# Kernel optimization log

Hardware: AMD Instinct MI355X
Metric: run time of the kernel (lower is better)

## Reference

```python
import jax, jax.numpy as jnp
import numpy as np

N, K, D_IN, D_H, D_A, N_CLS = 8192, 10, 1024, 512, 256, 4


def setup_inputs() -> dict:
    key = jax.random.key(0)
    ks = jax.random.split(key, 20)
    def lin(k, fan_in, shape):
        return jax.random.normal(k, shape, dtype=jnp.float32) / np.sqrt(fan_in)
    return {
        "x_path": jax.random.normal(ks[0], (N, D_IN), dtype=jnp.float32),
        "cluster_id": jax.random.randint(ks[1], (N,), 0, K),
        # per-cluster phi MLP (Linear 1024->512, ReLU, Linear 512->512, ReLU); dropout = eval identity
        "W1": lin(ks[2], D_IN, (K, D_IN, D_H)), "b1": jnp.zeros((K, D_H), jnp.float32),
        "W2": lin(ks[3], D_H, (K, D_H, D_H)), "b2": jnp.zeros((K, D_H), jnp.float32),
        # attention_net fc: Linear 512->512 + ReLU
        "fc_W": lin(ks[4], D_H, (D_H, D_H)), "fc_b": jnp.zeros((D_H,), jnp.float32),
        # Attn_Net_Gated: a=tanh(Va), b=sigmoid(Vb), A=(a*b)@Vc
        "Va": lin(ks[5], D_H, (D_H, D_A)), "ba": jnp.zeros((D_A,), jnp.float32),
        "Vb": lin(ks[6], D_H, (D_H, D_A)), "bb": jnp.zeros((D_A,), jnp.float32),
        "Vc": lin(ks[7], D_A, (D_A, 1)), "bc": jnp.zeros((1,), jnp.float32),
        # rho: Linear 512->256 + ReLU
        "rho_W": lin(ks[8], D_H, (D_H, D_A)), "rho_b": jnp.zeros((D_A,), jnp.float32),
        # classifier: Linear 256->4
        "cls_W": lin(ks[9], D_A, (D_A, N_CLS)), "cls_b": jnp.zeros((N_CLS,), jnp.float32),
    }


def reference(x_path, cluster_id, W1, b1, W2, b2, fc_W, fc_b,
              Va, ba, Vb, bb, Vc, bc, rho_W, rho_b, cls_W, cls_b):
    # mask[k, n] = 1 if patch n belongs to cluster k
    mask = (cluster_id[None, :] == jnp.arange(K)[:, None]).astype(x_path.dtype)  # [K, N]

    # per-cluster 2-layer MLP applied to all patches, masked mean-pool (= AdaptiveAvgPool1d(1))
    def phi(W1i, b1i, W2i, b2i):
        h = jax.nn.relu(x_path @ W1i + b1i)          # [N, 512]
        return jax.nn.relu(h @ W2i + b2i)            # [N, 512]
    y = jax.vmap(phi)(W1, b1, W2, b2)                # [K, N, 512]
    cnt = mask.sum(axis=1)                           # [K]
    pooled = jnp.einsum('kn,knd->kd', mask, y) / jnp.maximum(cnt, 1.0)[:, None]  # [K, 512]
    # empty cluster -> zeros (matches torch.zeros((1,512)) branch since b terms are zero via where)
    pooled = jnp.where(cnt[:, None] > 0, pooled, 0.0)

    # attention_net: fc + gated attention
    h = jax.nn.relu(pooled @ fc_W + fc_b)            # [K, 512]
    a = jnp.tanh(h @ Va + ba)                        # [K, 256]
    b = jax.nn.sigmoid(h @ Vb + bb)                  # [K, 256]
    A = (a * b) @ Vc + bc                            # [K, 1]
    A = jax.nn.softmax(A.T, axis=1)                  # [1, K]
    h_path = A @ h                                   # [1, 512]
    h_path = jax.nn.relu(h_path @ rho_W + rho_b)[0]  # [256]
    logits = (h_path @ cls_W + cls_b)[None, :]       # [1, 4]
    Y_hat = jnp.argmax(logits, axis=1, keepdims=True)
    hazards = jax.nn.sigmoid(logits)
    S = jnp.cumprod(1.0 - hazards, axis=1)
    return hazards, S, Y_hat
```

## Files before the change

kernel.cpp:

```cpp
#include <hip/hip_runtime.h>
#include <math.h>

#define NPATCH 8192
#define KC     10
#define DIN    1024
#define DH     512
#define DA     256
#define NCLS   4

#define TM  32
#define LDA 520

typedef unsigned short u16;
typedef short bf16x8 __attribute__((ext_vector_type(8)));
typedef float f32x4  __attribute__((ext_vector_type(4)));

#define OFF_CNT   0
#define OFF_BAR   48
#define OFF_IDX   64
#define OFF_PSUM  327744
#define OFF_H     348224
#define OFF_H2    368768
#define OFF_SRED  369792
#define OFF_W1P   373888
#define OFF_W2P   10859648

__device__ __forceinline__ u16 f2bf(float f) {
  union { float f; unsigned u; } v; v.f = f;
  unsigned r = (v.u + 0x7fffu + ((v.u >> 16) & 1u)) >> 16;
  return (u16)r;
}

__device__ __forceinline__ unsigned cvtpk(float lo, float hi) {
  unsigned r;
  asm("v_cvt_pk_bf16_f32 %0, %1, %2" : "=v"(r) : "v"(lo), "v"(hi));
  return r;
}

struct __align__(8) U16x4 { u16 x, y, z, w; };
union BF8U { bf16x8 v; unsigned u[4]; };

#define W1_TILES (KC * (DIN / 32) * (DH / 32))
#define W2_TILES (KC * (DH / 32) * (DH / 32))
#define NB_BUCKET 32
#define WT_PER_BLK 4
#define NB_PREP (NB_BUCKET + (W1_TILES + W2_TILES) / WT_PER_BLK)

__global__ __launch_bounds__(256) void prep_kernel(
    const int* __restrict__ cid, int* __restrict__ cnt,
    int* __restrict__ idxlist, const float* __restrict__ W1,
    const float* __restrict__ W2, u16* __restrict__ W1p,
    u16* __restrict__ W2p, float* __restrict__ psum) {
  int b = blockIdx.x, t = threadIdx.x;
  if (b < NB_BUCKET) {
    int g = b * 256 + t;
    if (g < KC * DH) psum[g] = 0.f;
    __shared__ int lcnt[KC], lbase[KC];
    if (t < KC) lcnt[t] = 0;
    __syncthreads();
    int n = b * 256 + t;
    int k = cid[n];
    int myoff = atomicAdd(&lcnt[k], 1);
    __syncthreads();
    if (t < KC) lbase[t] = atomicAdd(&cnt[t], lcnt[t]);
    __syncthreads();
    idxlist[k * NPATCH + lbase[k] + myoff] = n;
  } else {
    __shared__ u16 tile[32][33];
#pragma unroll
    for (int it = 0; it < WT_PER_BLK; ++it) {
      int bb = (b - NB_BUCKET) * WT_PER_BLK + it;
      const float* src;
      u16* dst;
      if (bb < W1_TILES) {
        int k = bb / 512, rem = bb % 512;
        int kb = rem / 16, n0 = (rem % 16) * 32;
        src = W1 + (size_t)k * DIN * DH + (size_t)kb * 32 * DH + n0;
        dst = W1p + (((size_t)(k * 32 + kb) * 512 + n0) * 32);
      } else {
        int b2 = bb - W1_TILES;
        int k = b2 / 256, rem = b2 % 256;
        int kb = rem / 16, n0 = (rem % 16) * 32;
        src = W2 + (size_t)k * DH * DH + (size_t)kb * 32 * DH + n0;
        dst = W2p + (((size_t)(k * 16 + kb) * 512 + n0) * 32);
      }
      {
        int ki = t >> 3, n4 = (t & 7) * 4;
        float4 v = *(const float4*)&src[(size_t)ki * DH + n4];
        tile[ki][n4 + 0] = f2bf(v.x);
        tile[ki][n4 + 1] = f2bf(v.y);
        tile[ki][n4 + 2] = f2bf(v.z);
        tile[ki][n4 + 3] = f2bf(v.w);
      }
      __syncthreads();
      {
        int n = t >> 3, ki = (t & 7) * 4;
        U16x4 o = {tile[ki + 0][n], tile[ki + 1][n], tile[ki + 2][n],
                   tile[ki + 3][n]};
        *(U16x4*)&dst[(size_t)n * 32 + ki] = o;
      }
      __syncthreads();
    }
  }
}

__global__ __launch_bounds__(512, 4) void phi_kernel(
    const float* __restrict__ x, const u16* __restrict__ W1p,
    const u16* __restrict__ W2p, const float* __restrict__ b1,
    const float* __restrict__ b2, const int* __restrict__ cnt,
    const int* __restrict__ idxlist, float* __restrict__ psum) {
  __shared__ __align__(16) u16 A0[TM * LDA];
  __shared__ __align__(16) u16 A1[TM * LDA];
  __shared__ int ridx[TM];

  const int tid = threadIdx.x;
  const int w = tid >> 6, lane = tid & 63;
  const int quad = lane >> 4, l16 = lane & 15;

  int cn[KC];
#pragma unroll
  for (int i = 0; i < KC; ++i) cn[i] = cnt[i];
  int G = 0;
#pragma unroll
  for (int i = 0; i < KC; ++i) G += (cn[i] + TM - 1) >> 5;

  const int s = blockIdx.x & 7, j = blockIdx.x >> 3;
  const int lo = (G * s) >> 3, hi = (G * (s + 1)) >> 3;

  for (int g = lo + j; g < hi; g += 64) {
    int kk = 0, rg = g, cntk = cn[0];
#pragma unroll
    for (int i = 0; i < KC - 1; ++i) {
      int nch = (cn[i] + TM - 1) >> 5;
      if (rg >= nch) { kk = i + 1; rg -= nch; cntk = cn[i + 1]; }
    }
    const int base = rg * TM;

    if (tid < TM)
      ridx[tid] = (base + tid < cntk) ? idxlist[kk * NPATCH + base + tid] : -1;
    __syncthreads();

    const u16* wb = W1p + ((size_t)(kk * 32) * 512 + (w * 64 + l16)) * 32 +
                    quad * 8;
    bf16x8 B[3][4];
#pragma unroll
    for (int p = 0; p < 3; ++p)
#pragma unroll
      for (int nt = 0; nt < 4; ++nt)
        B[p][nt] = *(const bf16x8*)(wb + (size_t)p * 16384 + nt * 512);

#pragma unroll
    for (int u8 = 0; u8 < 8; ++u8) {
      const int kh = u8 & 1;
      const int r = w * 4 + (u8 >> 1);
      int src = ridx[r];
      BF8U o;
      if (src >= 0) {
        const float4* xp =
            (const float4*)(x + (size_t)src * DIN + kh * 512 + lane * 8);
        float4 v0 = xp[0], v1 = xp[1];
        o.u[0] = cvtpk(v0.x, v0.y);
        o.u[1] = cvtpk(v0.z, v0.w);
        o.u[2] = cvtpk(v1.x, v1.y);
        o.u[3] = cvtpk(v1.z, v1.w);
      } else {
        o.u[0] = 0; o.u[1] = 0; o.u[2] = 0; o.u[3] = 0;
      }
      u16* dstbuf = kh ? A1 : A0;
      *(bf16x8*)&dstbuf[r * LDA + lane * 8] = o.v;
    }
    __syncthreads();

    const f32x4 zero4 = {0.f, 0.f, 0.f, 0.f};
    f32x4 acc[2][4];
#pragma unroll
    for (int m = 0; m < 2; ++m)
#pragma unroll
      for (int nt = 0; nt < 4; ++nt) acc[m][nt] = zero4;

#pragma unroll
    for (int ks = 0; ks < 32; ++ks) {
      const int cur = ks % 3;
      const u16* Abuf = (ks < 16) ? A0 : A1;
      const int ao = (ks & 15) * 32 + quad * 8;
      bf16x8 af0 = *(const bf16x8*)&Abuf[l16 * LDA + ao];
      bf16x8 af1 = *(const bf16x8*)&Abuf[(16 + l16) * LDA + ao];
#pragma unroll
      for (int nt = 0; nt < 4; ++nt) {
        acc[0][nt] = __builtin_amdgcn_mfma_f32_16x16x32_bf16(
            af0, B[cur][nt], acc[0][nt], 0, 0, 0);
        acc[1][nt] = __builtin_amdgcn_mfma_f32_16x16x32_bf16(
            af1, B[cur][nt], acc[1][nt], 0, 0, 0);
      }
      if (ks < 29) {
#pragma unroll
        for (int nt = 0; nt < 4; ++nt)
          B[cur][nt] =
              *(const bf16x8*)(wb + (size_t)(ks + 3) * 16384 + nt * 512);
      }
    }

    const u16* wb2 = W2p + ((size_t)(kk * 16) * 512 + (w * 64 + l16)) * 32 +
                     quad * 8;
#pragma unroll
    for (int p = 0; p < 3; ++p)
#pragma unroll
      for (int nt = 0; nt < 4; ++nt)
        B[p][nt] = *(const bf16x8*)(wb2 + (size_t)p * 16384 + nt * 512);

    __syncthreads();

#pragma unroll
    for (int m = 0; m < 2; ++m)
#pragma unroll
      for (int nt = 0; nt < 4; ++nt) {
        int c = w * 64 + nt * 16 + l16;
        float bias = b1[kk * DH + c];
#pragma unroll
        for (int r = 0; r < 4; ++r) {
          int row = m * 16 + quad * 4 + r;
          A0[row * LDA + c] = f2bf(fmaxf(acc[m][nt][r] + bias, 0.f));
        }
      }
    __syncthreads();

    f32x4 acc2[2][4];
#pragma unroll
    for (int m = 0; m < 2; ++m)
#pragma unroll
      for (int nt = 0; nt < 4; ++nt) acc2[m][nt] = zero4;

#pragma unroll
    for (int ks = 0; ks < 16; ++ks) {
      const int cur = ks % 3;
      const int ao = ks * 32 + quad * 8;
      bf16x8 af0 = *(const bf16x8*)&A0[l16 * LDA + ao];
      bf16x8 af1 = *(const bf16x8*)&A0[(16 + l16) * LDA + ao];
#pragma unroll
      for (int nt = 0; nt < 4; ++nt) {
        acc2[0][nt] = __builtin_amdgcn_mfma_f32_16x16x32_bf16(
            af0, B[cur][nt], acc2[0][nt], 0, 0, 0);
        acc2[1][nt] = __builtin_amdgcn_mfma_f32_16x16x32_bf16(
            af1, B[cur][nt], acc2[1][nt], 0, 0, 0);
      }
      if (ks < 13) {
#pragma unroll
        for (int nt = 0; nt < 4; ++nt)
          B[cur][nt] =
              *(const bf16x8*)(wb2 + (size_t)(ks + 3) * 16384 + nt * 512);
      }
    }

    float vmask[2][4];
#pragma unroll
    for (int m = 0; m < 2; ++m)
#pragma unroll
      for (int r = 0; r < 4; ++r)
        vmask[m][r] = (base + m * 16 + quad * 4 + r < cntk) ? 1.f : 0.f;

#pragma unroll
    for (int nt = 0; nt < 4; ++nt) {
      int col = w * 64 + nt * 16 + l16;
      float bias = b2[kk * DH + col];
      float sv = 0.f;
#pragma unroll
      for (int m = 0; m < 2; ++m)
#pragma unroll
        for (int r = 0; r < 4; ++r)
          sv += vmask[m][r] * fmaxf(acc2[m][nt][r] + bias, 0.f);
      sv += __shfl_xor(sv, 16, 64);
      sv += __shfl_xor(sv, 32, 64);
      if (quad == 0) atomicAdd(&psum[kk * DH + col], sv);
    }
  }
}

#define NTB 64

__device__ __forceinline__ void bar_arrive_wait(int* bar) {
  __syncthreads();
  if (threadIdx.x == 0) {
    __threadfence();
    __hip_atomic_fetch_add(bar, 1, __ATOMIC_RELEASE, __HIP_MEMORY_SCOPE_AGENT);
    while (__hip_atomic_load(bar, __ATOMIC_ACQUIRE,
                             __HIP_MEMORY_SCOPE_AGENT) < NTB) {
      __builtin_amdgcn_s_sleep(1);
    }
  }
  __syncthreads();
}

__global__ __launch_bounds__(256) void tail_kernel(
    const float* __restrict__ psum, const int* __restrict__ cnt,
    const float* __restrict__ fcW, const float* __restrict__ fcb,
    const float* __restrict__ Va, const float* __restrict__ ba,
    const float* __restrict__ Vb, const float* __restrict__ bb_,
    const float* __restrict__ Vc, const float* __restrict__ rhoW,
    const float* __restrict__ rhob, const float* __restrict__ clsW,
    const float* __restrict__ clsb, float* __restrict__ hstore,
    float* __restrict__ sred, float* __restrict__ h2g,
    int* __restrict__ bar, float* __restrict__ out) {
  __shared__ float p_sh[KC * DH];
  __shared__ float r1[2560];
  __shared__ float r2[2560];
  __shared__ float invs[KC];
  __shared__ float gate_sh[4 * KC];
  __shared__ float ws_sh[KC];
  __shared__ float hp_sh[DH];
  const int tid = threadIdx.x;
  const int b = blockIdx.x;

  if (tid < KC) {
    int c = cnt[tid];
    invs[tid] = (c > 0) ? 1.f / (float)c : 0.f;
  }
  __syncthreads();
#pragma unroll
  for (int it = 0; it < KC * DH / 256; ++it) {
    int e = it * 256 + tid;
    p_sh[e] = psum[e] * invs[e >> 9];
  }
  __syncthreads();
  {
    const int jj = tid & 7, dq = tid >> 3;
    const int j0 = b * 8;
    float acc[KC];
#pragma unroll
    for (int k = 0; k < KC; ++k) acc[k] = 0.f;
#pragma unroll 4
    for (int i = 0; i < 16; ++i) {
      int d = dq * 16 + i;
      float wv = fcW[(size_t)d * DH + j0 + jj];
#pragma unroll
      for (int k = 0; k < KC; ++k) acc[k] = fmaf(p_sh[k * DH + d], wv, acc[k]);
    }
#pragma unroll
    for (int k = 0; k < KC; ++k) r1[(dq * 8 + jj) * KC + k] = acc[k];
    __syncthreads();
    if (tid < 8 * KC) {
      int jj2 = tid / KC, k = tid % KC;
      float s = 0.f;
#pragma unroll
      for (int q = 0; q < 32; ++q) s += r1[(q * 8 + jj2) * KC + k];
      hstore[k * DH + j0 + jj2] = fmaxf(s + fcb[j0 + jj2], 0.f);
    }
  }
  bar_arrive_wait(&bar[0]);

#pragma unroll
  for (int it = 0; it < KC * DH / 256; ++it) {
    int e = it * 256 + tid;
    p_sh[e] = hstore[e];
  }
  __syncthreads();
  {
    const int jj = tid & 3, dq = tid >> 2;
    const int j0 = b * 4;
    float sa[KC], sb[KC];
#pragma unroll
    for (int k = 0; k < KC; ++k) { sa[k] = 0.f; sb[k] = 0.f; }
#pragma unroll 4
    for (int i = 0; i < 8; ++i) {
      int d = dq * 8 + i;
      float va = Va[(size_t)d * DA + j0 + jj];
      float vb = Vb[(size_t)d * DA + j0 + jj];
#pragma unroll
      for (int k = 0; k < KC; ++k) {
        float h = p_sh[k * DH + d];
        sa[k] = fmaf(h, va, sa[k]);
        sb[k] = fmaf(h, vb, sb[k]);
      }
    }
#pragma unroll
    for (int k = 0; k < KC; ++k) {
      r1[(dq * 4 + jj) * KC + k] = sa[k];
      r2[(dq * 4 + jj) * KC + k] = sb[k];
    }
    __syncthreads();
    if (tid < 4 * KC) {
      int jj2 = tid / KC, k = tid % KC;
      float ta = 0.f, tb = 0.f;
#pragma unroll
      for (int q = 0; q < 64; ++q) {
        ta += r1[(q * 4 + jj2) * KC + k];
        tb += r2[(q * 4 + jj2) * KC + k];
      }
      float a = tanhf(ta + ba[j0 + jj2]);
      float g = 1.f / (1.f + expf(-(tb + bb_[j0 + jj2])));
      gate_sh[jj2 * KC + k] = a * g * Vc[j0 + jj2];
    }
    __syncthreads();
    if (tid < KC) {
      float s = 0.f;
#pragma unroll
      for (int jj2 = 0; jj2 < 4; ++jj2) s += gate_sh[jj2 * KC + tid];
      sred[b * 16 + tid] = s;
    }
  }
  bar_arrive_wait(&bar[1]);

  if (tid < KC) {
    float s = 0.f;
    for (int q = 0; q < NTB; ++q) s += sred[q * 16 + tid];
    ws_sh[tid] = s;
  }
  __syncthreads();
  if (tid == 0) {
    float m = -1e30f;
#pragma unroll
    for (int k2 = 0; k2 < KC; ++k2) m = fmaxf(m, ws_sh[k2]);
    float Z = 0.f;
#pragma unroll
    for (int k2 = 0; k2 < KC; ++k2) {
      float e = expf(ws_sh[k2] - m);
      ws_sh[k2] = e;
      Z += e;
    }
    float iZ = 1.f / Z;
#pragma unroll
    for (int k2 = 0; k2 < KC; ++k2) ws_sh[k2] *= iZ;
  }
  __syncthreads();
#pragma unroll
  for (int it = 0; it < 2; ++it) {
    int d = it * 256 + tid;
    float s = 0.f;
#pragma unroll
    for (int k2 = 0; k2 < KC; ++k2) s = fmaf(ws_sh[k2], p_sh[k2 * DH + d], s);
    hp_sh[d] = s;
  }
  __syncthreads();
  {
    const int jj = tid & 3, dq = tid >> 2;
    const int j0 = b * 4;
    float acc = 0.f;
#pragma unroll 4
    for (int i = 0; i < 8; ++i) {
      int d = dq * 8 + i;
      acc = fmaf(hp_sh[d], rhoW[(size_t)d * DA + j0 + jj], acc);
    }
    r1[dq * 4 + jj] = acc;
    __syncthreads();
    if (tid < 4) {
      float s = 0.f;
#pragma unroll
      for (int q = 0; q < 64; ++q) s += r1[q * 4 + tid];
      h2g[j0 + tid] = fmaxf(s + rhob[j0 + tid], 0.f);
    }
  }

  if (b != 0) {
    __syncthreads();
    if (tid == 0) {
      __threadfence();
      __hip_atomic_fetch_add(&bar[2], 1, __ATOMIC_RELEASE,
                             __HIP_MEMORY_SCOPE_AGENT);
    }
    return;
  }
  bar_arrive_wait(&bar[2]);
  {
    float h = h2g[tid];
#pragma unroll
    for (int c = 0; c < NCLS; ++c)
      r1[c * 256 + tid] = h * clsW[(size_t)tid * NCLS + c];
    __syncthreads();
    for (int s = 128; s > 0; s >>= 1) {
      if (tid < s) {
#pragma unroll
        for (int c = 0; c < NCLS; ++c)
          r1[c * 256 + tid] += r1[c * 256 + tid + s];
      }
      __syncthreads();
    }
    if (tid == 0) {
      float lg[NCLS], hz[NCLS];
      int best = 0;
#pragma unroll
      for (int c = 0; c < NCLS; ++c) {
        lg[c] = r1[c * 256] + clsb[c];
        hz[c] = 1.f / (1.f + expf(-lg[c]));
        if (lg[c] > lg[best]) best = c;
      }
      float S = 1.f;
#pragma unroll
      for (int c = 0; c < NCLS; ++c) out[c] = hz[c];
#pragma unroll
      for (int c = 0; c < NCLS; ++c) {
        S *= (1.f - hz[c]);
        out[NCLS + c] = S;
      }
      out[2 * NCLS] = (float)best;
    }
  }
}

extern "C" void kernel_launch(void* const* d_in, const int* in_sizes, int n_in,
                              void* d_out, int out_size, void* d_ws,
                              size_t ws_size, hipStream_t stream) {
  const float* x    = (const float*)d_in[0];
  const int*   cid  = (const int*)d_in[1];
  const float* W1   = (const float*)d_in[2];
  const float* b1   = (const float*)d_in[3];
  const float* W2   = (const float*)d_in[4];
  const float* b2   = (const float*)d_in[5];
  const float* fcW  = (const float*)d_in[6];
  const float* fcb  = (const float*)d_in[7];
  const float* Va   = (const float*)d_in[8];
  const float* ba   = (const float*)d_in[9];
  const float* Vb   = (const float*)d_in[10];
  const float* bb_  = (const float*)d_in[11];
  const float* Vc   = (const float*)d_in[12];
  const float* rhoW = (const float*)d_in[14];
  const float* rhob = (const float*)d_in[15];
  const float* clsW = (const float*)d_in[16];
  const float* clsb = (const float*)d_in[17];
  float* out = (float*)d_out;

  char* ws = (char*)d_ws;
  int*   cnt     = (int*)(ws + OFF_CNT);
  int*   bar     = (int*)(ws + OFF_BAR);
  int*   idxlist = (int*)(ws + OFF_IDX);
  float* psum    = (float*)(ws + OFF_PSUM);
  float* hstore  = (float*)(ws + OFF_H);
  float* h2g     = (float*)(ws + OFF_H2);
  float* sred    = (float*)(ws + OFF_SRED);
  u16*   W1p     = (u16*)(ws + OFF_W1P);
  u16*   W2p     = (u16*)(ws + OFF_W2P);

  (void)hipMemsetAsync(cnt, 0, 64, stream);
  prep_kernel<<<NB_PREP, 256, 0, stream>>>(cid, cnt, idxlist, W1, W2, W1p, W2p,
                                           psum);
  phi_kernel<<<512, 512, 0, stream>>>(x, W1p, W2p, b1, b2, cnt, idxlist, psum);
  tail_kernel<<<NTB, 256, 0, stream>>>(psum, cnt, fcW, fcb, Va, ba, Vb, bb_,
                                       Vc, rhoW, rhob, clsW, clsb, hstore,
                                       sred, h2g, bar, out);
}
```

Measured before the change: 205.9 us.

## Stream phi weights via global_load_lds double buffer with swizzled LDS and rotated K order

Replaces the register-resident triple-buffered weight prefetch with direct global-to-LDS DMA (global_load_lds) into per-wave double buffers, using explicit vmcnt/lgkmcnt waits. The padded activation tiles become XOR-swizzled unpadded layouts, and each group starts the K loop at a group-dependent rotation to spread weight reads across blocks. It aims to cut VGPR pressure, which is why the occupancy hint in launch bounds is removed, and to overlap weight fetches with MFMA. The cost is extra LDS traffic and use and hand-tuned wait counts, which could be fragile.

```diff
diff --git a/kernel.cpp b/kernel.cpp
--- a/kernel.cpp
+++ b/kernel.cpp
@@ -9,7 +9,6 @@
 #define NCLS   4
 
 #define TM  32
-#define LDA 520
 
 typedef unsigned short u16;
 typedef short bf16x8 __attribute__((ext_vector_type(8)));
@@ -39,6 +38,12 @@
 
 struct __align__(8) U16x4 { u16 x, y, z, w; };
 union BF8U { bf16x8 v; unsigned u[4]; };
+
+__device__ __forceinline__ void dma16(const u16* gp, u16* lp) {
+  __builtin_amdgcn_global_load_lds(
+      (const __attribute__((address_space(1))) void*)gp,
+      (__attribute__((address_space(3))) void*)lp, 16, 0, 0);
+}
 
 #define W1_TILES (KC * (DIN / 32) * (DH / 32))
 #define W2_TILES (KC * (DH / 32) * (DH / 32))
@@ -104,19 +109,23 @@
   }
 }
 
-__global__ __launch_bounds__(512, 4) void phi_kernel(
+__global__ __launch_bounds__(512) void phi_kernel(
     const float* __restrict__ x, const u16* __restrict__ W1p,
     const u16* __restrict__ W2p, const float* __restrict__ b1,
     const float* __restrict__ b2, const int* __restrict__ cnt,
     const int* __restrict__ idxlist, float* __restrict__ psum) {
-  __shared__ __align__(16) u16 A0[TM * LDA];
-  __shared__ __align__(16) u16 A1[TM * LDA];
-  __shared__ int ridx[TM];
+  __shared__ __align__(16) u16 A0[TM * 512];
+  __shared__ __align__(16) u16 A1[TM * 512];
+  __shared__ __align__(16) u16 Bsh[2 * 8 * 4 * 512];
 
   const int tid = threadIdx.x;
   const int w = tid >> 6, lane = tid & 63;
   const int quad = lane >> 4, l16 = lane & 15;
 
+  const int boff = (w * 64 + l16) * 32 + quad * 8;
+  u16* myB0 = &Bsh[(size_t)w * 2048];
+  u16* myB1 = &Bsh[16384 + (size_t)w * 2048];
+
   int cn[KC];
 #pragma unroll
   for (int i = 0; i < KC; ++i) cn[i] = cnt[i];
@@ -135,27 +144,18 @@
       if (rg >= nch) { kk = i + 1; rg -= nch; cntk = cn[i + 1]; }
     }
     const int base = rg * TM;
-
-    if (tid < TM)
-      ridx[tid] = (base + tid < cntk) ? idxlist[kk * NPATCH + base + tid] : -1;
-    __syncthreads();
-
-    const u16* wb = W1p + ((size_t)(kk * 32) * 512 + (w * 64 + l16)) * 32 +
-                    quad * 8;
-    bf16x8 B[3][4];
-#pragma unroll
-    for (int p = 0; p < 3; ++p)
-#pragma unroll
-      for (int nt = 0; nt < 4; ++nt)
-        B[p][nt] = *(const bf16x8*)(wb + (size_t)p * 16384 + nt * 512);
+    const int rot = (g * 5) & 31;
+    const int rot2 = (g * 5) & 15;
+
+    __syncthreads();
 
 #pragma unroll
     for (int u8 = 0; u8 < 8; ++u8) {
       const int kh = u8 & 1;
       const int r = w * 4 + (u8 >> 1);
-      int src = ridx[r];
       BF8U o;
-      if (src >= 0) {
+      if (base + r < cntk) {
+        int src = idxlist[kk * NPATCH + base + r];
         const float4* xp =
             (const float4*)(x + (size_t)src * DIN + kh * 512 + lane * 8);
         float4 v0 = xp[0], v1 = xp[1];
@@ -167,9 +167,19 @@
         o.u[0] = 0; o.u[1] = 0; o.u[2] = 0; o.u[3] = 0;
       }
       u16* dstbuf = kh ? A1 : A0;
-      *(bf16x8*)&dstbuf[r * LDA + lane * 8] = o.v;
-    }
-    __syncthreads();
+      *(bf16x8*)&dstbuf[r * 512 + (lane ^ (r & 7)) * 8] = o.v;
+    }
+    __syncthreads();
+
+    const u16* w1base = W1p + (size_t)(kk * 32) * 16384 + boff;
+    const u16* w2base = W2p + (size_t)(kk * 16) * 16384 + boff;
+#pragma unroll
+    for (int p = 0; p < 2; ++p) {
+      const u16* sb = w1base + (size_t)(((p + rot) & 31)) * 16384;
+      u16* lb = p ? myB1 : myB0;
+#pragma unroll
+      for (int nt = 0; nt < 4; ++nt) dma16(sb + nt * 512, lb + nt * 512);
+    }
 
     const f32x4 zero4 = {0.f, 0.f, 0.f, 0.f};
     f32x4 acc[2][4];
@@ -179,35 +189,37 @@
       for (int nt = 0; nt < 4; ++nt) acc[m][nt] = zero4;
 
 #pragma unroll
-    for (int ks = 0; ks < 32; ++ks) {
-      const int cur = ks % 3;
-      const u16* Abuf = (ks < 16) ? A0 : A1;
-      const int ao = (ks & 15) * 32 + quad * 8;
-      bf16x8 af0 = *(const bf16x8*)&Abuf[l16 * LDA + ao];
-      bf16x8 af1 = *(const bf16x8*)&Abuf[(16 + l16) * LDA + ao];
+    for (int t = 0; t < 32; ++t) {
+      asm volatile("s_waitcnt vmcnt(4)" ::: "memory");
+      __builtin_amdgcn_sched_barrier(0);
+      const u16* mb = (t & 1) ? myB1 : myB0;
+      bf16x8 bf[4];
+#pragma unroll
+      for (int nt = 0; nt < 4; ++nt)
+        bf[nt] = *(const bf16x8*)(mb + nt * 512 + lane * 8);
+      const int ks = (t + rot) & 31;
+      const u16* Ab = (ks < 16) ? A0 : A1;
+      const int c8 = (((ks & 15) * 4 + quad) ^ (l16 & 7)) * 8;
+      bf16x8 af0 = *(const bf16x8*)&Ab[l16 * 512 + c8];
+      bf16x8 af1 = *(const bf16x8*)&Ab[(16 + l16) * 512 + c8];
+      asm volatile("s_waitcnt lgkmcnt(0)" ::: "memory");
+      __builtin_amdgcn_sched_barrier(0);
+      {
+        u16* lb = (t & 1) ? myB1 : myB0;
+        const u16* sb = (t < 30)
+            ? w1base + (size_t)(((t + 2 + rot) & 31)) * 16384
+            : w2base + (size_t)(((t - 30 + rot2) & 15)) * 16384;
+#pragma unroll
+        for (int nt = 0; nt < 4; ++nt) dma16(sb + nt * 512, lb + nt * 512);
+      }
 #pragma unroll
       for (int nt = 0; nt < 4; ++nt) {
         acc[0][nt] = __builtin_amdgcn_mfma_f32_16x16x32_bf16(
-            af0, B[cur][nt], acc[0][nt], 0, 0, 0);
+            af0, bf[nt], acc[0][nt], 0, 0, 0);
         acc[1][nt] = __builtin_amdgcn_mfma_f32_16x16x32_bf16(
-            af1, B[cur][nt], acc[1][nt], 0, 0, 0);
-      }
-      if (ks < 29) {
-#pragma unroll
-        for (int nt = 0; nt < 4; ++nt)
-          B[cur][nt] =
-              *(const bf16x8*)(wb + (size_t)(ks + 3) * 16384 + nt * 512);
-      }
-    }
-
-    const u16* wb2 = W2p + ((size_t)(kk * 16) * 512 + (w * 64 + l16)) * 32 +
-                     quad * 8;
-#pragma unroll
-    for (int p = 0; p < 3; ++p)
-#pragma unroll
-      for (int nt = 0; nt < 4; ++nt)
-        B[p][nt] = *(const bf16x8*)(wb2 + (size_t)p * 16384 + nt * 512);
-
+            af1, bf[nt], acc[1][nt], 0, 0, 0);
+      }
+    }
     __syncthreads();
 
 #pragma unroll
@@ -219,7 +231,8 @@
 #pragma unroll
         for (int r = 0; r < 4; ++r) {
           int row = m * 16 + quad * 4 + r;
-          A0[row * LDA + c] = f2bf(fmaxf(acc[m][nt][r] + bias, 0.f));
+          A0[row * 512 + (((c >> 3) ^ (row & 7)) * 8) + (c & 7)] =
+              f2bf(fmaxf(acc[m][nt][r] + bias, 0.f));
         }
       }
     __syncthreads();
@@ -231,23 +244,36 @@
       for (int nt = 0; nt < 4; ++nt) acc2[m][nt] = zero4;
 
 #pragma unroll
-    for (int ks = 0; ks < 16; ++ks) {
-      const int cur = ks % 3;
-      const int ao = ks * 32 + quad * 8;
-      bf16x8 af0 = *(const bf16x8*)&A0[l16 * LDA + ao];
-      bf16x8 af1 = *(const bf16x8*)&A0[(16 + l16) * LDA + ao];
+    for (int t = 0; t < 16; ++t) {
+      if (t == 15) {
+        asm volatile("s_waitcnt vmcnt(0)" ::: "memory");
+      } else {
+        asm volatile("s_waitcnt vmcnt(4)" ::: "memory");
+      }
+      __builtin_amdgcn_sched_barrier(0);
+      const u16* mb = (t & 1) ? myB1 : myB0;
+      bf16x8 bf[4];
+#pragma unroll
+      for (int nt = 0; nt < 4; ++nt)
+        bf[nt] = *(const bf16x8*)(mb + nt * 512 + lane * 8);
+      const int ks2 = (t + rot2) & 15;
+      const int c8 = ((ks2 * 4 + quad) ^ (l16 & 7)) * 8;
+      bf16x8 af0 = *(const bf16x8*)&A0[l16 * 512 + c8];
+      bf16x8 af1 = *(const bf16x8*)&A0[(16 + l16) * 512 + c8];
+      asm volatile("s_waitcnt lgkmcnt(0)" ::: "memory");
+      __builtin_amdgcn_sched_barrier(0);
+      if (t < 14) {
+        u16* lb = (t & 1) ? myB1 : myB0;
+        const u16* sb = w2base + (size_t)(((t + 2 + rot2) & 15)) * 16384;
+#pragma unroll
+        for (int nt = 0; nt < 4; ++nt) dma16(sb + nt * 512, lb + nt * 512);
+      }
 #pragma unroll
       for (int nt = 0; nt < 4; ++nt) {
         acc2[0][nt] = __builtin_amdgcn_mfma_f32_16x16x32_bf16(
-            af0, B[cur][nt], acc2[0][nt], 0, 0, 0);
+            af0, bf[nt], acc2[0][nt], 0, 0, 0);
         acc2[1][nt] = __builtin_amdgcn_mfma_f32_16x16x32_bf16(
-            af1, B[cur][nt], acc2[1][nt], 0, 0, 0);
-      }
-      if (ks < 13) {
-#pragma unroll
-        for (int nt = 0; nt < 4; ++nt)
-          B[cur][nt] =
-              *(const bf16x8*)(wb2 + (size_t)(ks + 3) * 16384 + nt * 512);
+            af1, bf[nt], acc2[1][nt], 0, 0, 0);
       }
     }
 
```

New measurement: 211.4 us. 1.03x slower.

## Pre-convert x to bf16 and DMA rows into LDS via global_load_lds

Applied to the files above, without the earlier changes.

The prep kernel gains a pass that converts x to bf16 in workspace, and the phi kernel loads activation rows straight into shared memory with global_load_lds instead of loading fp32 and converting in registers. The packed weight layout is reordered so each lane's 16-byte B fragment is contiguous across the wave, giving coalesced weight loads. Weight-packing blocks now handle one tile each instead of four. This adds an extra full read and write of x in prep, in exchange for halving the bytes phi reads for x and removing conversion work from the GEMM kernel.

```diff
diff --git a/kernel.cpp b/kernel.cpp
--- a/kernel.cpp
+++ b/kernel.cpp
@@ -24,6 +24,7 @@
 #define OFF_SRED  369792
 #define OFF_W1P   373888
 #define OFF_W2P   10859648
+#define OFF_XB    16102528
 
 __device__ __forceinline__ u16 f2bf(float f) {
   union { float f; unsigned u; } v; v.f = f;
@@ -31,26 +32,26 @@
   return (u16)r;
 }
 
-__device__ __forceinline__ unsigned cvtpk(float lo, float hi) {
-  unsigned r;
-  asm("v_cvt_pk_bf16_f32 %0, %1, %2" : "=v"(r) : "v"(lo), "v"(hi));
-  return r;
-}
-
 struct __align__(8) U16x4 { u16 x, y, z, w; };
-union BF8U { bf16x8 v; unsigned u[4]; };
+
+__device__ __forceinline__ void dma16(const u16* gp, void* lp) {
+  __builtin_amdgcn_global_load_lds(
+      (const __attribute__((address_space(1))) void*)gp,
+      (__attribute__((address_space(3))) void*)lp, 16, 0, 0);
+}
 
 #define W1_TILES (KC * (DIN / 32) * (DH / 32))
 #define W2_TILES (KC * (DH / 32) * (DH / 32))
 #define NB_BUCKET 32
-#define WT_PER_BLK 4
-#define NB_PREP (NB_BUCKET + (W1_TILES + W2_TILES) / WT_PER_BLK)
+#define NB_XB     2048
+#define NB_PREP (NB_BUCKET + NB_XB + W1_TILES + W2_TILES)
 
 __global__ __launch_bounds__(256) void prep_kernel(
     const int* __restrict__ cid, int* __restrict__ cnt,
     int* __restrict__ idxlist, const float* __restrict__ W1,
     const float* __restrict__ W2, u16* __restrict__ W1p,
-    u16* __restrict__ W2p, float* __restrict__ psum) {
+    u16* __restrict__ W2p, const float* __restrict__ x,
+    u16* __restrict__ xb, float* __restrict__ psum) {
   int b = blockIdx.x, t = threadIdx.x;
   if (b < NB_BUCKET) {
     int g = b * 256 + t;
@@ -65,47 +66,55 @@
     if (t < KC) lbase[t] = atomicAdd(&cnt[t], lcnt[t]);
     __syncthreads();
     idxlist[k * NPATCH + lbase[k] + myoff] = n;
+  } else if (b < NB_BUCKET + NB_XB) {
+    int cb = b - NB_BUCKET;
+    size_t basei = (size_t)cb * 4096;
+#pragma unroll
+    for (int i = 0; i < 4; ++i) {
+      size_t off = basei + (size_t)i * 1024 + (size_t)t * 4;
+      float4 v = *(const float4*)(x + off);
+      U16x4 o = {f2bf(v.x), f2bf(v.y), f2bf(v.z), f2bf(v.w)};
+      *(U16x4*)(xb + off) = o;
+    }
   } else {
     __shared__ u16 tile[32][33];
-#pragma unroll
-    for (int it = 0; it < WT_PER_BLK; ++it) {
-      int bb = (b - NB_BUCKET) * WT_PER_BLK + it;
-      const float* src;
-      u16* dst;
-      if (bb < W1_TILES) {
-        int k = bb / 512, rem = bb % 512;
-        int kb = rem / 16, n0 = (rem % 16) * 32;
-        src = W1 + (size_t)k * DIN * DH + (size_t)kb * 32 * DH + n0;
-        dst = W1p + (((size_t)(k * 32 + kb) * 512 + n0) * 32);
-      } else {
-        int b2 = bb - W1_TILES;
-        int k = b2 / 256, rem = b2 % 256;
-        int kb = rem / 16, n0 = (rem % 16) * 32;
-        src = W2 + (size_t)k * DH * DH + (size_t)kb * 32 * DH + n0;
-        dst = W2p + (((size_t)(k * 16 + kb) * 512 + n0) * 32);
-      }
-      {
-        int ki = t >> 3, n4 = (t & 7) * 4;
-        float4 v = *(const float4*)&src[(size_t)ki * DH + n4];
-        tile[ki][n4 + 0] = f2bf(v.x);
-        tile[ki][n4 + 1] = f2bf(v.y);
-        tile[ki][n4 + 2] = f2bf(v.z);
-        tile[ki][n4 + 3] = f2bf(v.w);
-      }
-      __syncthreads();
-      {
-        int n = t >> 3, ki = (t & 7) * 4;
-        U16x4 o = {tile[ki + 0][n], tile[ki + 1][n], tile[ki + 2][n],
-                   tile[ki + 3][n]};
-        *(U16x4*)&dst[(size_t)n * 32 + ki] = o;
-      }
-      __syncthreads();
+    int bb = b - NB_BUCKET - NB_XB;
+    const float* src;
+    u16* dst;
+    if (bb < W1_TILES) {
+      int k = bb / 512, rem = bb % 512;
+      int kb = rem / 16, n0 = (rem % 16) * 32;
+      src = W1 + (size_t)k * DIN * DH + (size_t)kb * 32 * DH + n0;
+      dst = W1p + (((size_t)(k * 32 + kb) * 512 + n0) * 32);
+    } else {
+      int b2 = bb - W1_TILES;
+      int k = b2 / 256, rem = b2 % 256;
+      int kb = rem / 16, n0 = (rem % 16) * 32;
+      src = W2 + (size_t)k * DH * DH + (size_t)kb * 32 * DH + n0;
+      dst = W2p + (((size_t)(k * 16 + kb) * 512 + n0) * 32);
+    }
+    {
+      int ki = t >> 3, n4 = (t & 7) * 4;
+      float4 v = *(const float4*)&src[(size_t)ki * DH + n4];
+      tile[ki][n4 + 0] = f2bf(v.x);
+      tile[ki][n4 + 1] = f2bf(v.y);
+      tile[ki][n4 + 2] = f2bf(v.z);
+      tile[ki][n4 + 3] = f2bf(v.w);
+    }
+    __syncthreads();
+    {
+      int n = t >> 3, ki = (t & 7) * 4;
+      U16x4 o = {tile[ki + 0][n], tile[ki + 1][n], tile[ki + 2][n],
+                 tile[ki + 3][n]};
+      size_t idx = (size_t)(n >> 4) * 512 + ((ki >> 3) * 128) +
+                   ((n & 15) * 8) + (ki & 7);
+      *(U16x4*)&dst[idx] = o;
     }
   }
 }
 
 __global__ __launch_bounds__(512, 4) void phi_kernel(
-    const float* __restrict__ x, const u16* __restrict__ W1p,
+    const u16* __restrict__ xb, const u16* __restrict__ W1p,
     const u16* __restrict__ W2p, const float* __restrict__ b1,
     const float* __restrict__ b2, const int* __restrict__ cnt,
     const int* __restrict__ idxlist, float* __restrict__ psum) {
@@ -140,8 +149,7 @@
       ridx[tid] = (base + tid < cntk) ? idxlist[kk * NPATCH + base + tid] : -1;
     __syncthreads();
 
-    const u16* wb = W1p + ((size_t)(kk * 32) * 512 + (w * 64 + l16)) * 32 +
-                    quad * 8;
+    const u16* wb = W1p + (size_t)(kk * 32) * 16384 + w * 2048 + lane * 8;
     bf16x8 B[3][4];
 #pragma unroll
     for (int p = 0; p < 3; ++p)
@@ -154,20 +162,14 @@
       const int kh = u8 & 1;
       const int r = w * 4 + (u8 >> 1);
       int src = ridx[r];
-      BF8U o;
+      u16* dstbuf = kh ? A1 : A0;
       if (src >= 0) {
-        const float4* xp =
-            (const float4*)(x + (size_t)src * DIN + kh * 512 + lane * 8);
-        float4 v0 = xp[0], v1 = xp[1];
-        o.u[0] = cvtpk(v0.x, v0.y);
-        o.u[1] = cvtpk(v0.z, v0.w);
-        o.u[2] = cvtpk(v1.x, v1.y);
-        o.u[3] = cvtpk(v1.z, v1.w);
+        dma16(xb + (size_t)src * DIN + kh * 512 + lane * 8,
+              &dstbuf[r * LDA]);
       } else {
-        o.u[0] = 0; o.u[1] = 0; o.u[2] = 0; o.u[3] = 0;
-      }
-      u16* dstbuf = kh ? A1 : A0;
-      *(bf16x8*)&dstbuf[r * LDA + lane * 8] = o.v;
+        bf16x8 z = {0, 0, 0, 0, 0, 0, 0, 0};
+        *(bf16x8*)&dstbuf[r * LDA + lane * 8] = z;
+      }
     }
     __syncthreads();
 
@@ -179,10 +181,10 @@
       for (int nt = 0; nt < 4; ++nt) acc[m][nt] = zero4;
 
 #pragma unroll
-    for (int ks = 0; ks < 32; ++ks) {
-      const int cur = ks % 3;
-      const u16* Abuf = (ks < 16) ? A0 : A1;
-      const int ao = (ks & 15) * 32 + quad * 8;
+    for (int t = 0; t < 32; ++t) {
+      const int cur = t % 3;
+      const u16* Abuf = (t < 16) ? A0 : A1;
+      const int ao = (t & 15) * 32 + quad * 8;
       bf16x8 af0 = *(const bf16x8*)&Abuf[l16 * LDA + ao];
       bf16x8 af1 = *(const bf16x8*)&Abuf[(16 + l16) * LDA + ao];
 #pragma unroll
@@ -192,16 +194,15 @@
         acc[1][nt] = __builtin_amdgcn_mfma_f32_16x16x32_bf16(
             af1, B[cur][nt], acc[1][nt], 0, 0, 0);
       }
-      if (ks < 29) {
+      if (t < 29) {
 #pragma unroll
         for (int nt = 0; nt < 4; ++nt)
           B[cur][nt] =
-              *(const bf16x8*)(wb + (size_t)(ks + 3) * 16384 + nt * 512);
-      }
-    }
-
-    const u16* wb2 = W2p + ((size_t)(kk * 16) * 512 + (w * 64 + l16)) * 32 +
-                     quad * 8;
+              *(const bf16x8*)(wb + (size_t)(t + 3) * 16384 + nt * 512);
+      }
+    }
+
+    const u16* wb2 = W2p + (size_t)(kk * 16) * 16384 + w * 2048 + lane * 8;
 #pragma unroll
     for (int p = 0; p < 3; ++p)
 #pragma unroll
@@ -231,9 +232,9 @@
       for (int nt = 0; nt < 4; ++nt) acc2[m][nt] = zero4;
 
 #pragma unroll
-    for (int ks = 0; ks < 16; ++ks) {
-      const int cur = ks % 3;
-      const int ao = ks * 32 + quad * 8;
+    for (int t = 0; t < 16; ++t) {
+      const int cur = t % 3;
+      const int ao = t * 32 + quad * 8;
       bf16x8 af0 = *(const bf16x8*)&A0[l16 * LDA + ao];
       bf16x8 af1 = *(const bf16x8*)&A0[(16 + l16) * LDA + ao];
 #pragma unroll
@@ -243,11 +244,11 @@
         acc2[1][nt] = __builtin_amdgcn_mfma_f32_16x16x32_bf16(
             af1, B[cur][nt], acc2[1][nt], 0, 0, 0);
       }
-      if (ks < 13) {
+      if (t < 13) {
 #pragma unroll
         for (int nt = 0; nt < 4; ++nt)
           B[cur][nt] =
-              *(const bf16x8*)(wb2 + (size_t)(ks + 3) * 16384 + nt * 512);
+              *(const bf16x8*)(wb2 + (size_t)(t + 3) * 16384 + nt * 512);
       }
     }
 
@@ -527,11 +528,13 @@
   float* sred    = (float*)(ws + OFF_SRED);
   u16*   W1p     = (u16*)(ws + OFF_W1P);
   u16*   W2p     = (u16*)(ws + OFF_W2P);
+  u16*   xb      = (u16*)(ws + OFF_XB);
 
   (void)hipMemsetAsync(cnt, 0, 64, stream);
   prep_kernel<<<NB_PREP, 256, 0, stream>>>(cid, cnt, idxlist, W1, W2, W1p, W2p,
-                                           psum);
-  phi_kernel<<<512, 512, 0, stream>>>(x, W1p, W2p, b1, b2, cnt, idxlist, psum);
+                                           x, xb, psum);
+  phi_kernel<<<512, 512, 0, stream>>>(xb, W1p, W2p, b1, b2, cnt, idxlist,
+                                      psum);
   tail_kernel<<<NTB, 256, 0, stream>>>(psum, cnt, fcW, fcb, Va, ba, Vb, bb_,
                                        Vc, rhoW, rhob, clsW, clsb, hstore,
                                        sred, h2g, bar, out);
```

New measurement: 190.7 us. -7.4%, faster.
